# Kernel optimization log

Measured on AMD Instinct MI355X. Metric: run time of the kernel, lower is better.

The kernel has to match this reference:

```python
import jax, jax.numpy as jnp
import numpy as np

IMG_H, IMG_W = 800, 1216
STRIDES = [4, 8, 16, 32, 64]
SIZES = [32, 64, 128, 256, 512]
RATIOS = (2.0, 1.0, 0.5)
LVTOP = 1000     # per-level top-k
IMTOP = 1000     # image-level top-k
IOU_THR = 0.7
MIN_SIZE = 0.001
BBOX_CLIP = float(np.log(1000.0 / 16.0))  # dw/dh clamp, matches decode=(1,1,log(1000/16))


def conv2d(x, w, b, pad):
    y = jax.lax.conv_general_dilated(x, w, (1, 1), [(pad, pad), (pad, pad)],
                                     dimension_numbers=('NCHW', 'OIHW', 'NCHW'))
    return y + b[None, :, None, None]


def head_level(x, conv_w, conv_b, cls_w, cls_b, reg_w, reg_b):
    # ConvUnit 3x3 + plain ReLU (no BN), then 1x1 reg/cls heads
    B = x.shape[0]
    h = jax.nn.relu(conv2d(x, conv_w, conv_b, 1))
    reg = conv2d(h, reg_w, reg_b, 0).transpose(0, 2, 3, 1).reshape(B, -1, 4)      # [B,H*W*A,4]
    scr = jax.nn.sigmoid(conv2d(h, cls_w, cls_b, 0).transpose(0, 2, 3, 1).reshape(B, -1))  # [B,H*W*A]
    return reg, scr


def make_priors(H, W, stride, size):
    # rounded base anchors (1 scale x 3 ratios), corner-aligned grid (xyxy)
    r = jnp.array(RATIOS, dtype=jnp.float32)
    hr = jnp.sqrt(r)
    ws, hs = size / hr, size * hr
    base = jnp.round(jnp.stack([-ws / 2, -hs / 2, ws / 2, hs / 2], axis=1))  # [A,4]
    ys, xs = jnp.meshgrid(jnp.arange(H) * stride, jnp.arange(W) * stride, indexing='ij')
    shift = jnp.stack([xs, ys, xs, ys], -1).reshape(-1, 1, 4).astype(jnp.float32)
    return (shift + base[None]).reshape(-1, 4)  # [H*W*A,4], order matches head reshape


def decode(reg, priors):
    pw = priors[..., 2] - priors[..., 0]
    ph = priors[..., 3] - priors[..., 1]
    pcx = priors[..., 0] + 0.5 * pw
    pcy = priors[..., 1] + 0.5 * ph
    dx, dy = reg[..., 0], reg[..., 1]
    dw = jnp.minimum(reg[..., 2], BBOX_CLIP)
    dh = jnp.minimum(reg[..., 3], BBOX_CLIP)
    cx, cy = dx * pw + pcx, dy * ph + pcy
    w, h = jnp.exp(dw) * pw, jnp.exp(dh) * ph
    return jnp.stack([cx - 0.5 * w, cy - 0.5 * h, cx + 0.5 * w, cy + 0.5 * h], -1)


def nms_keep(boxes, scores):
    # greedy NMS; boxes [K,4] sorted by score desc, scores < -0.5 mark invalid/padding
    K = boxes.shape[0]
    area = (boxes[:, 2] - boxes[:, 0]) * (boxes[:, 3] - boxes[:, 1])
    lt = jnp.maximum(boxes[:, None, :2], boxes[None, :, :2])
    rb = jnp.minimum(boxes[:, None, 2:], boxes[None, :, 2:])
    wh = jnp.clip(rb - lt, 0.0)
    inter = wh[..., 0] * wh[..., 1]
    iou = inter / jnp.maximum(area[:, None] + area[None, :] - inter, 1e-9)
    iou = jax.lax.stop_gradient(iou)  # selection is discrete
    idx = jnp.arange(K)

    def step(keep, xs):
        row, i = xs
        sup = keep[i] & (row > IOU_THR) & (idx > i)
        return keep & ~sup, None

    keep, _ = jax.lax.scan(step, scores > -0.5, (iou, idx))
    return keep


def process_level(reg, scr, priors):
    B, N = scr.shape
    k = min(LVTOP, N)
    topv, topi = jax.lax.top_k(scr, k)                              # [B,k], sorted desc
    reg_s = jnp.take_along_axis(reg, topi[..., None], axis=1)       # [B,k,4]
    boxes = decode(reg_s, priors[topi])
    boxes = jnp.stack([
        jnp.clip(boxes[..., 0], 0.0, IMG_W), jnp.clip(boxes[..., 1], 0.0, IMG_H),
        jnp.clip(boxes[..., 2], 0.0, IMG_W), jnp.clip(boxes[..., 3], 0.0, IMG_H)], -1)
    w = boxes[..., 2] - boxes[..., 0]
    h = boxes[..., 3] - boxes[..., 1]
    sc = jnp.where((w > MIN_SIZE) & (h > MIN_SIZE), topv, -1.0)     # drop tiny boxes
    if k < LVTOP:  # pad small levels (e.g. P6) to a fixed candidate count
        boxes = jnp.pad(boxes, ((0, 0), (0, LVTOP - k), (0, 0)))
        sc = jnp.pad(sc, ((0, 0), (0, LVTOP - k)), constant_values=-1.0)
    keep = jax.vmap(nms_keep)(boxes, sc)                            # per-level NMS
    return boxes, jnp.where(keep, sc, -1.0)


def forward(p2, p3, p4, p5, p6, conv_w, conv_b, cls_w, cls_b, reg_w, reg_b):
    levels = [p2, p3, p4, p5, p6]
    all_boxes, all_scores = [], []
    for lvl, stride, size in zip(levels, STRIDES, SIZES):
        reg, scr = head_level(lvl, conv_w, conv_b, cls_w, cls_b, reg_w, reg_b)
        priors = make_priors(lvl.shape[2], lvl.shape[3], stride, size)
        b, s = process_level(reg, scr, priors)
        all_boxes.append(b)
        all_scores.append(s)
    boxes = jnp.concatenate(all_boxes, axis=1)
    scores = jnp.concatenate(all_scores, axis=1)
    fv, fi = jax.lax.top_k(scores, IMTOP)                           # image-level top-k
    fb = jnp.take_along_axis(boxes, fi[..., None], axis=1)
    return jnp.concatenate([fb, fv[..., None]], axis=-1)            # [B, IMTOP, 5]


def setup_inputs():
    key = jax.random.key(0)
    ks = jax.random.split(key, 8)
    C = 256
    shapes = [(2, C, 200, 304), (2, C, 100, 152), (2, C, 50, 76), (2, C, 25, 38), (2, C, 13, 19)]
    inp = {}
    for i, (name, sh) in enumerate(zip(['p2', 'p3', 'p4', 'p5', 'p6'], shapes)):
        inp[name] = jax.random.normal(ks[i], sh, dtype=jnp.float32)
    inp['conv_w'] = jax.random.normal(ks[5], (C, C, 3, 3), dtype=jnp.float32) * 0.02
    inp['conv_b'] = jnp.zeros((C,), dtype=jnp.float32)
    inp['cls_w'] = jax.random.normal(ks[6], (3, C, 1, 1), dtype=jnp.float32) * 0.02
    inp['cls_b'] = jnp.zeros((3,), dtype=jnp.float32)
    inp['reg_w'] = jax.random.normal(ks[7], (12, C, 1, 1), dtype=jnp.float32) * 0.01
    inp['reg_b'] = jnp.zeros((12,), dtype=jnp.float32)
    return inp


def reference(p2, p3, p4, p5, p6, conv_w, conv_b, cls_w, cls_b, reg_w, reg_b):
    return forward(p2, p3, p4, p5, p6, conv_w, conv_b, cls_w, cls_b, reg_w, reg_b)
```

## Files before the change

### kernel.cpp

```cpp
#include <hip/hip_runtime.h>
#include <stdint.h>
#include <math.h>

typedef unsigned long long u64;
typedef unsigned int u32;
typedef unsigned char u8;
typedef short s16x8 __attribute__((ext_vector_type(8)));
typedef float f32x4 __attribute__((ext_vector_type(4)));

#define ATOT 242991
#define PXTOT 80997
#define PXPAD 82971

__device__ __constant__ int    d_Hs[5]      = {200,100,50,25,13};
__device__ __constant__ int    d_Ws[5]      = {304,152,76,38,19};
__device__ __constant__ int    d_Wp[5]      = {306,154,78,40,21};
__device__ __constant__ int    d_stridec[5] = {4,8,16,32,64};
__device__ __constant__ double d_sized[5]   = {32.0,64.0,128.0,256.0,512.0};
__device__ __constant__ int    d_off[5]     = {0,182400,228000,239400,242250};
__device__ __constant__ int    d_pxoff[6]   = {0,60800,76000,79800,80750,80997};
__device__ __constant__ int    d_poff[5]    = {0,61812,77520,81576,82656};
__device__ __constant__ int    d_Ncand[5]   = {182400,45600,11400,2850,741};
__device__ __constant__ int    d_xcb[5]     = {0,1900,2375,2494,2524};
__device__ __constant__ int    d_ctb[5]     = {0,1000,1300,1400,1425};
__device__ __constant__ int    d_tX[5]      = {5,3,2,1,1};

__device__ __forceinline__ u32 f2k32(float f) {
  u32 u = __float_as_uint(f);
  return (u & 0x80000000u) ? ~u : (u | 0x80000000u);
}
__device__ __forceinline__ float k2f32(u32 k) {
  u32 u = (k & 0x80000000u) ? (k & 0x7FFFFFFFu) : ~k;
  return __uint_as_float(u);
}
__device__ __forceinline__ u64 d2k(double d) {
  u64 b = (u64)__double_as_longlong(d);
  return (b & 0x8000000000000000ull) ? ~b : (b | 0x8000000000000000ull);
}
__device__ __forceinline__ unsigned short f2bf(float v) {
  u32 b = __float_as_uint(v);
  return (unsigned short)((b + 0x7FFFu + ((b >> 16) & 1u)) >> 16);
}
__device__ __forceinline__ float bf2f(unsigned short h) {
  return __uint_as_float(((u32)h) << 16);
}

__global__ void wtrans_k(const float* __restrict__ w, float* __restrict__ wt) {
  int gid = blockIdx.x * 256 + threadIdx.x;
  if (gid >= 2304 * 256) return;
  int oc = gid & 255;
  int rest = gid >> 8;
  int ic = rest / 9, tap = rest % 9;
  wt[gid] = w[(oc * 256 + ic) * 9 + tap];
}

__global__ void wcvt_k(const float* __restrict__ w, short* __restrict__ wbh,
                       short* __restrict__ wbl) {
  int gid = blockIdx.x * 256 + threadIdx.x;
  if (gid >= 73728) return;
  int lane = gid & 63;
  int rest = gid >> 6;
  int oct = rest & 15, rs = rest >> 4;
  int slice = rs & 7, tap = rs >> 3;
  int oc = oct * 16 + (lane & 15);
  int icb = slice * 32 + (lane >> 4) * 8;
  size_t ob = (size_t)gid * 8;
#pragma unroll
  for (int j = 0; j < 8; ++j) {
    float v = w[(oc * 256 + icb + j) * 9 + tap];
    unsigned short h = f2bf(v);
    wbh[ob + j] = (short)h;
    wbl[ob + j] = (short)f2bf(v - bf2f(h));
  }
}

__global__ __launch_bounds__(256) void xcvt_k(
    const float* __restrict__ x0, const float* __restrict__ x1,
    const float* __restrict__ x2, const float* __restrict__ x3,
    const float* __restrict__ x4, short* __restrict__ xh, short* __restrict__ xl)
{
  __shared__ float tile[32 * 257];
  const int bid = blockIdx.x;
  const int b = bid / 2532;
  int r = bid % 2532;
  int lvl = 0;
#pragma unroll
  for (int l2 = 1; l2 < 5; ++l2) if (r >= d_xcb[l2]) lvl = l2;
  const int chunk = r - d_xcb[lvl];
  const int H = d_Hs[lvl], W = d_Ws[lvl], HW = H * W, Wp = d_Wp[lvl];
  const int px0 = chunk * 32;
  const float* xs[5] = {x0, x1, x2, x3, x4};
  const float* xb = xs[lvl] + (size_t)b * 256 * HW;
  const int t = threadIdx.x;

  for (int icg = 0; icg < 32; ++icg) {
    int ic = icg * 8 + (t >> 5);
    int px = px0 + (t & 31);
    float v = (px < HW) ? xb[(size_t)ic * HW + px] : 0.f;
    tile[(t & 31) * 257 + ic] = v;
  }
  __syncthreads();
  int px = t >> 3;
  int gpx = px0 + px;
  if (gpx < HW) {
    int yy = gpx / W, xx = gpx % W;
    size_t obase = ((size_t)(b * PXPAD + d_poff[lvl]) +
                    (size_t)(yy + 1) * Wp + (xx + 1)) * 256 + (size_t)(t & 7) * 32;
#pragma unroll
    for (int q = 0; q < 4; ++q) {
      s16x8 hi, lo;
#pragma unroll
      for (int j = 0; j < 8; ++j) {
        u32 bits = __float_as_uint(tile[px * 257 + (t & 7) * 32 + q * 8 + j]);
        hi[j] = (short)(bits >> 16);
        lo[j] = (short)(bits & 0xFFFFu);
      }
      *(s16x8*)(xh + obase + q * 8) = hi;
      *(s16x8*)(xl + obase + q * 8) = lo;
    }
  }
}

__global__ __launch_bounds__(256) void conv_mfma_k(
    const short* __restrict__ xh,
    const short* __restrict__ wbh, const short* __restrict__ wbl,
    const float* __restrict__ convb, const float* __restrict__ clsw,
    const float* __restrict__ clsb, float* __restrict__ scr32)
{
  __shared__ float zl[4][64][3];
  const int bid = blockIdx.x;
  const int b = bid / 1438;
  int r = bid % 1438;
  int lvl = 0;
#pragma unroll
  for (int l2 = 1; l2 < 5; ++l2) if (r >= d_ctb[l2]) lvl = l2;
  const int lid = r - d_ctb[lvl];
  const int tX = d_tX[lvl];
  const int y = lid / tX, x0 = (lid % tX) * 64;
  const int W = d_Ws[lvl], Wp = d_Wp[lvl];
  const size_t pbase = (size_t)(b * PXPAD + d_poff[lvl]);

  const int t = threadIdx.x;
  const int lane = t & 63;
  const int wid = t >> 6;
  const int aoff = (lane & 15) * 256 + (lane >> 4) * 8;

  f32x4 acc[4][4];
#pragma unroll
  for (int m = 0; m < 4; ++m)
#pragma unroll
    for (int o = 0; o < 4; ++o) acc[m][o] = (f32x4){0.f, 0.f, 0.f, 0.f};

#pragma unroll 1
  for (int tap = 0; tap < 9; ++tap) {
    const int ky = tap / 3, kx = tap % 3;
    const size_t re = (pbase + (size_t)(y + ky) * Wp + (x0 + kx)) * 256;
    const short* pa = xh + re;
    const short* pbh = wbh + (size_t)tap * 8 * 16 * 512;
    const short* pbl = wbl + (size_t)tap * 8 * 16 * 512;
#pragma unroll 1
    for (int slice = 0; slice < 8; ++slice) {
      s16x8 bh[4], bl4[4], a[4];
#pragma unroll
      for (int o = 0; o < 4; ++o) {
        size_t bo = ((size_t)(slice * 16 + wid * 4 + o) * 64 + lane) * 8;
        bh[o]  = *(const s16x8*)(pbh + bo);
        bl4[o] = *(const s16x8*)(pbl + bo);
      }
#pragma unroll
      for (int m = 0; m < 4; ++m) {
        size_t ao = (size_t)aoff + slice * 32 + m * 4096;
        a[m] = *(const s16x8*)(pa + ao);
      }
#pragma unroll
      for (int m = 0; m < 4; ++m)
#pragma unroll
        for (int o = 0; o < 4; ++o) {
          acc[m][o] = __builtin_amdgcn_mfma_f32_16x16x32_bf16(a[m], bh[o],  acc[m][o], 0, 0, 0);
          acc[m][o] = __builtin_amdgcn_mfma_f32_16x16x32_bf16(a[m], bl4[o], acc[m][o], 0, 0, 0);
        }
    }
  }

  float bb[4], cw0[4], cw1[4], cw2[4];
#pragma unroll
  for (int o = 0; o < 4; ++o) {
    int oc = wid * 64 + o * 16 + (lane & 15);
    bb[o]  = convb[oc];
    cw0[o] = clsw[0 * 256 + oc];
    cw1[o] = clsw[1 * 256 + oc];
    cw2[o] = clsw[2 * 256 + oc];
  }
#pragma unroll
  for (int m = 0; m < 4; ++m) {
#pragma unroll
    for (int q = 0; q < 4; ++q) {
      float h0 = fmaxf(acc[m][0][q] + bb[0], 0.f);
      float h1 = fmaxf(acc[m][1][q] + bb[1], 0.f);
      float h2 = fmaxf(acc[m][2][q] + bb[2], 0.f);
      float h3 = fmaxf(acc[m][3][q] + bb[3], 0.f);
      float z0 = fmaf(h0, cw0[0], fmaf(h1, cw0[1], fmaf(h2, cw0[2], h3 * cw0[3])));
      float z1 = fmaf(h0, cw1[0], fmaf(h1, cw1[1], fmaf(h2, cw1[2], h3 * cw1[3])));
      float z2 = fmaf(h0, cw2[0], fmaf(h1, cw2[1], fmaf(h2, cw2[2], h3 * cw2[3])));
      z0 += __shfl_xor(z0, 1); z0 += __shfl_xor(z0, 2); z0 += __shfl_xor(z0, 4); z0 += __shfl_xor(z0, 8);
      z1 += __shfl_xor(z1, 1); z1 += __shfl_xor(z1, 2); z1 += __shfl_xor(z1, 4); z1 += __shfl_xor(z1, 8);
      z2 += __shfl_xor(z2, 1); z2 += __shfl_xor(z2, 2); z2 += __shfl_xor(z2, 4); z2 += __shfl_xor(z2, 8);
      if ((lane & 15) == 0) {
        int slot = m * 16 + (lane >> 4) * 4 + q;
        zl[wid][slot][0] = z0; zl[wid][slot][1] = z1; zl[wid][slot][2] = z2;
      }
    }
  }
  __syncthreads();
  if (t < 192) {
    int slot = t / 3, head = t % 3;
    int col = x0 + slot;
    if (col < W) {
      float z = zl[0][slot][head] + zl[1][slot][head] + zl[2][slot][head] +
                zl[3][slot][head] + clsb[head];
      int pix = y * W + col;
      scr32[(size_t)b * ATOT + d_off[lvl] + (size_t)pix * 3 + head] =
          1.f / (1.f + expf(-z));
    }
  }
}

__device__ __forceinline__ void locate(int gid, int& b, int& r, int& lvl) {
  b = gid / ATOT; r = gid % ATOT;
  lvl = (r < 182400) ? 0 : (r < 228000) ? 1 : (r < 239400) ? 2 : (r < 242250) ? 3 : 4;
}

__global__ void hist_hi_k(const float* __restrict__ scr, u32* __restrict__ hist) {
  int gid = blockIdx.x * 256 + threadIdx.x;
  if (gid >= 2 * ATOT) return;
  int b, r, lvl; locate(gid, b, r, lvl);
  u32 key = f2k32(scr[gid]);
  atomicAdd(&hist[((b * 5 + lvl) << 16) + (key >> 16)], 1u);
}

__global__ void scan_hi_k(const u32* __restrict__ hist, int* __restrict__ meta) {
  int bl = blockIdx.x, lvl = bl % 5;
  u32 k_sel = (u32)min(1000, d_Ncand[lvl]);
  const u32* h = hist + ((size_t)bl << 16);
  __shared__ u32 part[256];
  __shared__ u32 row[256];
  __shared__ int csel;
  __shared__ u32 cumsh;
  int t = threadIdx.x;
  u32 s = 0;
  for (int v = 0; v < 256; ++v) s += h[t * 256 + v];
  part[t] = s;
  __syncthreads();
  if (t == 0) {
    u32 cum = 0; int c = 255;
    for (; c > 0; --c) { if (cum + part[c] >= k_sel) break; cum += part[c]; }
    csel = c; cumsh = cum;
  }
  __syncthreads();
  row[t] = h[csel * 256 + t];
  __syncthreads();
  if (t == 0) {
    u32 cum = cumsh;
    int pivot = csel * 256;
    for (int v = 255; v >= 0; --v) {
      if (cum + row[v] >= k_sel) { pivot = csel * 256 + v; break; }
      cum += row[v];
    }
    meta[bl * 8 + 0] = pivot;
    meta[bl * 8 + 1] = (int)cum;
  }
}

__global__ void hist_lo_k(const float* __restrict__ scr, const int* __restrict__ meta,
                          u32* __restrict__ hist) {
  int gid = blockIdx.x * 256 + threadIdx.x;
  if (gid >= 2 * ATOT) return;
  int b, r, lvl; locate(gid, b, r, lvl);
  int bl = b * 5 + lvl;
  u32 key = f2k32(scr[gid]);
  if ((int)(key >> 16) == meta[bl * 8 + 0])
    atomicAdd(&hist[(bl << 16) + (key & 0xFFFFu)], 1u);
}

__global__ void scan_lo_k(const u32* __restrict__ hist, int* __restrict__ meta) {
  int bl = blockIdx.x, lvl = bl % 5;
  u32 k_sel = (u32)min(1000, d_Ncand[lvl]);
  const u32* h = hist + ((size_t)bl << 16);
  __shared__ u32 part[256];
  __shared__ u32 row[256];
  __shared__ int csel;
  __shared__ u32 cumsh;
  int t = threadIdx.x;
  u32 s = 0;
  for (int v = 0; v < 256; ++v) s += h[t * 256 + v];
  part[t] = s;
  __syncthreads();
  if (t == 0) {
    u32 cum = (u32)meta[bl * 8 + 1];
    int c = 255;
    for (; c > 0; --c) { if (cum + part[c] >= k_sel) break; cum += part[c]; }
    csel = c; cumsh = cum;
  }
  __syncthreads();
  row[t] = h[csel * 256 + t];
  __syncthreads();
  if (t == 0) {
    u32 cum = cumsh;
    int pivot = csel * 256;
    for (int v = 255; v >= 0; --v) {
      if (cum + row[v] >= k_sel) { pivot = csel * 256 + v; break; }
      cum += row[v];
    }
    u32 P = (((u32)meta[bl * 8 + 0]) << 16) | (u32)pivot;
    u32 T = f2k32(k2f32(P) - 5e-3f);
    if (d_Ncand[lvl] <= 1000) T = 0;
    meta[bl * 8 + 2] = (int)T;
    meta[bl * 8 + 4] = 0;
  }
}

__global__ void compact_k(const float* __restrict__ scr, int* __restrict__ meta,
                          u32* __restrict__ complist, u8* __restrict__ flags) {
  int gid = blockIdx.x * 256 + threadIdx.x;
  if (gid >= 2 * ATOT) return;
  int b, r, lvl; locate(gid, b, r, lvl);
  int bl = b * 5 + lvl;
  u32 key = f2k32(scr[gid]);
  if (key >= (u32)meta[bl * 8 + 2]) {
    int pos = atomicAdd(&meta[bl * 8 + 4], 1);
    if (pos < 8192) {
      u32 li = (u32)(r - d_off[lvl]);
      complist[bl * 8192 + pos] = li;
      flags[b * PXTOT + d_pxoff[lvl] + li / 3] = 1;
    }
  }
}

__global__ void pxcompact_k(u8* __restrict__ flags, u32* __restrict__ worklist,
                            int* __restrict__ wlcount) {
  int gid = blockIdx.x * 256 + threadIdx.x;
  if (gid >= 2 * PXTOT) return;
  if (flags[gid]) {
    flags[gid] = 0;
    int pos = atomicAdd(wlcount, 1);
    if (pos < 65536) worklist[pos] = (u32)gid;
  }
}

#define RSG 2048
__global__ __launch_bounds__(256) void rescore_k(
    const short* __restrict__ xh, const short* __restrict__ xl,
    const float* __restrict__ wt, const float* __restrict__ convb,
    const float* __restrict__ clsw, const float* __restrict__ clsb,
    const float* __restrict__ regw, const float* __restrict__ regb,
    const u32* __restrict__ worklist, const int* __restrict__ wlcount,
    double* __restrict__ scr64, double* __restrict__ reg64)
{
  __shared__ float xlb[4 * 2304];
  __shared__ double hl[4 * 256];
  const int t = threadIdx.x;
  int count = *wlcount; if (count > 65536) count = 65536;

  for (int base = blockIdx.x * 4; base < count; base += RSG * 4) {
    int sb[4], slvl[4], spix[4];
    size_t pb0[4];
    bool valid[4];
#pragma unroll
    for (int s = 0; s < 4; ++s) {
      int w = base + s;
      valid[s] = (w < count);
      sb[s] = 0; slvl[s] = 0; spix[s] = 0; pb0[s] = 0;
      if (valid[s]) {
        u32 g = worklist[w];
        int b = (int)(g / PXTOT), lp = (int)(g % PXTOT);
        int lvl = 0;
#pragma unroll
        for (int l = 1; l < 5; ++l) if (lp >= d_pxoff[l]) lvl = l;
        int pix = lp - d_pxoff[lvl];
        int W = d_Ws[lvl], Wp = d_Wp[lvl];
        int py = pix / W, px = pix % W;
        sb[s] = b; slvl[s] = lvl; spix[s] = pix;
        pb0[s] = ((size_t)(b * PXPAD + d_poff[lvl]) + (size_t)py * Wp + px) * 256;
      }
    }
    __syncthreads();
#pragma unroll
    for (int s = 0; s < 4; ++s) {
      if (valid[s]) {
        int Wp = d_Wp[slvl[s]];
        for (int i = t; i < 1152; i += 256) {
          int tap = i >> 7, pair = i & 127;
          int ky = tap / 3, kx = tap % 3;
          size_t po = pb0[s] + ((size_t)ky * Wp + kx) * 256 + (size_t)pair * 2;
          u32 vh = *(const u32*)(xh + po);
          u32 vl = *(const u32*)(xl + po);
          float xa  = __uint_as_float(((vh & 0xFFFFu) << 16) | (vl & 0xFFFFu));
          float xb2 = __uint_as_float((vh & 0xFFFF0000u) | (vl >> 16));
          xlb[s * 2304 + (pair * 2) * 9 + tap] = xa;
          xlb[s * 2304 + (pair * 2 + 1) * 9 + tap] = xb2;
        }
      }
    }
    __syncthreads();
    double h[4] = {0.0, 0.0, 0.0, 0.0};
    for (int ic = 0; ic < 256; ++ic) {
      double wd[9];
#pragma unroll
      for (int tap = 0; tap < 9; ++tap)
        wd[tap] = (double)wt[(ic * 9 + tap) * 256 + t];
#pragma unroll
      for (int s = 0; s < 4; ++s) {
        const float* xp = &xlb[s * 2304 + ic * 9];
#pragma unroll
        for (int tap = 0; tap < 9; ++tap)
          h[s] = fma((double)xp[tap], wd[tap], h[s]);
      }
    }
    double bias = (double)convb[t];
#pragma unroll
    for (int s = 0; s < 4; ++s) {
      h[s] = fmax(h[s] + bias, 0.0);
      hl[s * 256 + t] = h[s];
    }
    __syncthreads();
    {
      int s = t >> 6, lane = t & 63;
      if (valid[s]) {
        int lvl = slvl[s];
        size_t g3 = (size_t)sb[s] * ATOT + d_off[lvl] + (size_t)spix[s] * 3;
        for (int head = 0; head < 15; ++head) {
          const float* hw = (head < 3) ? (clsw + head * 256) : (regw + (head - 3) * 256);
          double part = 0.0;
#pragma unroll
          for (int q = 0; q < 4; ++q) {
            int oc = lane + q * 64;
            part = fma(hl[s * 256 + oc], (double)hw[oc], part);
          }
          part += __shfl_xor(part, 32);
          part += __shfl_xor(part, 16);
          part += __shfl_xor(part, 8);
          part += __shfl_xor(part, 4);
          part += __shfl_xor(part, 2);
          part += __shfl_xor(part, 1);
          if (lane == 0) {
            double z = part + (double)((head < 3) ? clsb[head] : regb[head - 3]);
            if (head < 3) scr64[g3 + head] = 1.0 / (1.0 + exp(-z));
            else { int hh = head - 3; reg64[(g3 + (hh >> 2)) * 4 + (hh & 3)] = z; }
          }
        }
      }
    }
    __syncthreads();
  }
}

__global__ void buildkeys_k(const u32* __restrict__ complist, const int* __restrict__ meta,
                            const double* __restrict__ scr64, u64* __restrict__ comp64) {
  int bl = blockIdx.x;
  int b = bl / 5, lvl = bl % 5;
  int M = meta[bl * 8 + 4]; if (M > 8192) M = 8192;
  for (int i = threadIdx.x; i < 8192; i += 256) {
    u64 key = 0;
    if (i < M) {
      u32 li = complist[bl * 8192 + i];
      double sc = scr64[(size_t)b * ATOT + d_off[lvl] + li];
      key = ((d2k(sc) >> 18) << 18) | (u64)(0x3FFFFu - li);
    }
    comp64[bl * 8192 + i] = key;
  }
}

__device__ void bitonic8192_desc(u64* s) {
  int t = threadIdx.x;
  for (int k = 2; k <= 8192; k <<= 1) {
    for (int j = k >> 1; j > 0; j >>= 1) {
      __syncthreads();
#pragma unroll
      for (int q = 0; q < 4; ++q) {
        int i = t + q * 1024;
        int l = (i << 1) - (i & (j - 1));
        int m = l + j;
        bool up = ((l & k) == 0);
        u64 a = s[l], bb = s[m];
        if ((a < bb) == up) { s[l] = bb; s[m] = a; }
      }
    }
  }
  __syncthreads();
}

__global__ __launch_bounds__(1024) void sort_level_k(const u64* __restrict__ comp64,
                                                     const int* __restrict__ meta,
                                                     int* __restrict__ topidx) {
  int bl = blockIdx.x, lvl = bl % 5;
  int k_sel = min(1000, d_Ncand[lvl]);
  __shared__ u64 s[8192];
  int M = meta[bl * 8 + 4]; if (M > 8192) M = 8192;
  for (int i = threadIdx.x; i < 8192; i += 1024)
    s[i] = (i < M) ? comp64[bl * 8192 + i] : 0ull;
  __syncthreads();
  bitonic8192_desc(s);
  for (int r = threadIdx.x; r < 1000; r += 1024) {
    int v = -1;
    if (r < k_sel && r < M) v = (int)(0x3FFFFu - (u32)(s[r] & 0x3FFFFu));
    topidx[bl * 1000 + r] = v;
  }
}

__global__ void decode_k(const int* __restrict__ topidx, const double* __restrict__ scr64,
                         const double* __restrict__ reg64, double* __restrict__ boxes,
                         double* __restrict__ sc0) {
  int gid = blockIdx.x * 256 + threadIdx.x;
  if (gid >= 10000) return;
  int bl = gid / 1000, rank = gid % 1000;
  int b = bl / 5, lvl = bl % 5;
  int idx = topidx[bl * 1000 + rank];
  double X1 = 0.0, Y1 = 0.0, X2 = 0.0, Y2 = 0.0, sc = -1.0;
  if (idx >= 0) {
    size_t g = (size_t)b * ATOT + d_off[lvl] + idx;
    double s = scr64[g];
    double dx = reg64[g * 4 + 0], dy = reg64[g * 4 + 1];
    const double BCLIP = 4.135166556742356;
    double dw = fmin(reg64[g * 4 + 2], BCLIP);
    double dh = fmin(reg64[g * 4 + 3], BCLIP);
    int a = idx % 3, pix = idx / 3;
    int W = d_Ws[lvl];
    int py = pix / W, px = pix % W;
    double r = (a == 0) ? 2.0 : (a == 1) ? 1.0 : 0.5;
    double hr = sqrt(r);
    double size = d_sized[lvl];
    double wsz = size / hr, hsz = size * hr;
    double bx2 = rint(wsz * 0.5), by2 = rint(hsz * 0.5);
    double bx1 = rint(-(wsz * 0.5)), by1 = rint(-(hsz * 0.5));
    double sx = (double)(px * d_stridec[lvl]), sy = (double)(py * d_stridec[lvl]);
    double x1 = sx + bx1, yy1 = sy + by1;
    double x2 = sx + bx2, yy2 = sy + by2;
    double pw = x2 - x1, ph = yy2 - yy1;
    double pcx = x1 + 0.5 * pw, pcy = yy1 + 0.5 * ph;
    double cx = dx * pw + pcx, cy = dy * ph + pcy;
    double w = exp(dw) * pw, h = exp(dh) * ph;
    X1 = fmin(fmax(cx - 0.5 * w, 0.0), 1216.0);
    Y1 = fmin(fmax(cy - 0.5 * h, 0.0), 800.0);
    X2 = fmin(fmax(cx + 0.5 * w, 0.0), 1216.0);
    Y2 = fmin(fmax(cy + 0.5 * h, 0.0), 800.0);
    sc = ((X2 - X1) > 0.001 && (Y2 - Y1) > 0.001) ? s : -1.0;
  }
  double* bp = boxes + (size_t)(bl * 1000 + rank) * 4;
  bp[0] = X1; bp[1] = Y1; bp[2] = X2; bp[3] = Y2;
  sc0[bl * 1000 + rank] = sc;
}

__global__ __launch_bounds__(256) void nms_mask_k(const double* __restrict__ boxes,
                                                  u64* __restrict__ gmask) {
  int blk = blockIdx.x;
  int bl = blk >> 2, qt = blk & 3;
  __shared__ double X1[1000], Y1[1000], X2[1000], Y2[1000], AR[1000];
  int t = threadIdx.x;
  for (int i = t; i < 1000; i += 256) {
    const double* bp = boxes + (size_t)(bl * 1000 + i) * 4;
    double x1 = bp[0], y1 = bp[1], x2 = bp[2], y2 = bp[3];
    X1[i] = x1; Y1[i] = y1; X2[i] = x2; Y2[i] = y2;
    AR[i] = (x2 - x1) * (y2 - y1);
  }
  __syncthreads();
  if (t < 250) {
    int i = qt * 250 + t;
    double ax1 = X1[i], ay1 = Y1[i], ax2 = X2[i], ay2 = Y2[i], aa = AR[i];
    u64* gm = gmask + (size_t)bl * 16000 + (size_t)i * 16;
    for (int wj = 0; wj < 16; ++wj) {
      u64 bits = 0;
      int jb0 = wj * 64;
      for (int jb = 0; jb < 64; ++jb) {
        int j = jb0 + jb;
        if (j <= i || j >= 1000) continue;
        double lx = fmax(ax1, X1[j]), ly = fmax(ay1, Y1[j]);
        double rx = fmin(ax2, X2[j]), ry = fmin(ay2, Y2[j]);
        double ww = fmax(rx - lx, 0.0), hh = fmax(ry - ly, 0.0);
        double inter = ww * hh;
        double uni = (aa + AR[j]) - inter;
        double iou = inter / fmax(uni, 1e-9);
        if (iou > 0.7) bits |= (1ull << jb);
      }
      gm[wj] = bits;
    }
  }
}

__global__ void nms_scan_k(double* __restrict__ sc0, const u64* __restrict__ gmask) {
  int bl = blockIdx.x;
  int lane = threadIdx.x;
  const u64* gm = gmask + (size_t)bl * 16000;
  u64 keepw = 0;
  if (lane < 16) {
    for (int jb = 0; jb < 64; ++jb) {
      int j = lane * 64 + jb;
      if (j < 1000 && sc0[bl * 1000 + j] > -0.5) keepw |= (1ull << jb);
    }
  }
  u64 m0 = 0, m1 = 0, m2 = 0, m3 = 0;
  if (lane < 16) {
    m0 = gm[0 * 16 + lane]; m1 = gm[1 * 16 + lane];
    m2 = gm[2 * 16 + lane]; m3 = gm[3 * 16 + lane];
  }
  for (int i = 0; i < 1000; i += 4) {
    u64 n0 = 0, n1 = 0, n2 = 0, n3 = 0;
    if (lane < 16 && i + 4 < 1000) {
      n0 = gm[(i + 4) * 16 + lane]; n1 = gm[(i + 5) * 16 + lane];
      n2 = gm[(i + 6) * 16 + lane]; n3 = gm[(i + 7) * 16 + lane];
    }
    { u64 kw = __shfl(keepw, (i    ) >> 6); if ((kw >> ((i    ) & 63)) & 1) { if (lane < 16) keepw &= ~m0; } }
    { u64 kw = __shfl(keepw, (i + 1) >> 6); if ((kw >> ((i + 1) & 63)) & 1) { if (lane < 16) keepw &= ~m1; } }
    { u64 kw = __shfl(keepw, (i + 2) >> 6); if ((kw >> ((i + 2) & 63)) & 1) { if (lane < 16) keepw &= ~m2; } }
    { u64 kw = __shfl(keepw, (i + 3) >> 6); if ((kw >> ((i + 3) & 63)) & 1) { if (lane < 16) keepw &= ~m3; } }
    m0 = n0; m1 = n1; m2 = n2; m3 = n3;
  }
  if (lane < 16) {
    for (int jb = 0; jb < 64; ++jb) {
      int j = lane * 64 + jb;
      if (j < 1000) {
        double ss = sc0[bl * 1000 + j];
        sc0[bl * 1000 + j] = ((keepw >> jb) & 1) ? ss : -1.0;
      }
    }
  }
}

__global__ __launch_bounds__(1024) void final_k(const double* __restrict__ sc0,
                                                const double* __restrict__ boxes,
                                                float* __restrict__ out) {
  int b = blockIdx.x;
  __shared__ u64 s[8192];
  for (int i = threadIdx.x; i < 8192; i += 1024) {
    u64 v = 0;
    if (i < 5000) {
      u64 k = d2k(sc0[b * 5000 + i]);
      v = ((k >> 18) << 18) | (u64)(0x3FFFFu - (u32)i);
    }
    s[i] = v;
  }
  __syncthreads();
  bitonic8192_desc(s);
  for (int r = threadIdx.x; r < 1000; r += 1024) {
    u64 v = s[r];
    int idx = (int)(0x3FFFFu - (u32)(v & 0x3FFFFu));
    double score = sc0[b * 5000 + idx];
    const double* bp = boxes + (size_t)(b * 5000 + idx) * 4;
    float* op = out + ((size_t)b * 1000 + r) * 5;
    op[0] = (float)bp[0]; op[1] = (float)bp[1];
    op[2] = (float)bp[2]; op[3] = (float)bp[3];
    op[4] = (float)score;
  }
}

extern "C" void kernel_launch(void* const* d_in, const int* in_sizes, int n_in,
                              void* d_out, int out_size, void* d_ws, size_t ws_size,
                              hipStream_t stream) {
  const float* p[5];
  for (int i = 0; i < 5; ++i) p[i] = (const float*)d_in[i];
  const float* conv_w = (const float*)d_in[5];
  const float* conv_b = (const float*)d_in[6];
  const float* cls_w  = (const float*)d_in[7];
  const float* cls_b  = (const float*)d_in[8];
  const float* reg_w  = (const float*)d_in[9];
  const float* reg_b  = (const float*)d_in[10];
  float* out = (float*)d_out;

  char* ws = (char*)d_ws;
  size_t off = 0;
  auto alloc = [&](size_t bytes) -> void* {
    void* pt = ws + off;
    off = (off + bytes + 255) & ~(size_t)255;
    return pt;
  };
  const size_t XTB = (size_t)2 * PXPAD * 256 * 2 + 65536;
  float*  wt       = (float*) alloc(2304ull * 256 * 4);
  short*  wbh      = (short*) alloc(73728ull * 8 * 2);
  short*  wbl      = (short*) alloc(73728ull * 8 * 2);
  short*  xh       = (short*) alloc(XTB);
  short*  xl       = (short*) alloc(XTB);
  float*  scr32    = (float*) alloc(2ull * ATOT * 4);
  double* scr64    = (double*)alloc(2ull * ATOT * 8);
  double* reg64    = (double*)alloc(2ull * ATOT * 4 * 8);
  u32*    hist     = (u32*)   alloc(10ull * 65536 * 4);
  int*    meta     = (int*)   alloc(10ull * 8 * 4);
  u32*    complist = (u32*)   alloc(10ull * 8192 * 4);
  u64*    comp64   = (u64*)   alloc(10ull * 8192 * 8);
  u8*     flags    = (u8*)    alloc(2ull * PXTOT);
  u32*    worklist = (u32*)   alloc(65536ull * 4);
  int*    wlcount  = (int*)   alloc(256);
  int*    topidx   = (int*)   alloc(10ull * 1000 * 4);
  double* boxes    = (double*)alloc(2ull * 5000 * 4 * 8);
  double* sc0      = (double*)alloc(2ull * 5000 * 8);
  u64*    gmask    = (u64*)   alloc(10ull * 1000 * 16 * 8);

  wtrans_k<<<(2304 * 256 + 255) / 256, 256, 0, stream>>>(conv_w, wt);
  wcvt_k<<<288, 256, 0, stream>>>(conv_w, wbh, wbl);
  hipMemsetAsync(xh, 0, XTB, stream);
  hipMemsetAsync(xl, 0, XTB, stream);
  xcvt_k<<<5064, 256, 0, stream>>>(p[0], p[1], p[2], p[3], p[4], xh, xl);
  conv_mfma_k<<<2876, 256, 0, stream>>>(xh, wbh, wbl, conv_b, cls_w, cls_b, scr32);

  int nblk = (2 * ATOT + 255) / 256;
  hipMemsetAsync(hist, 0, 10ull * 65536 * 4, stream);
  hist_hi_k<<<nblk, 256, 0, stream>>>(scr32, hist);
  scan_hi_k<<<10, 256, 0, stream>>>(hist, meta);
  hipMemsetAsync(hist, 0, 10ull * 65536 * 4, stream);
  hist_lo_k<<<nblk, 256, 0, stream>>>(scr32, meta, hist);
  scan_lo_k<<<10, 256, 0, stream>>>(hist, meta);

  hipMemsetAsync(flags, 0, 2ull * PXTOT, stream);
  hipMemsetAsync(wlcount, 0, 4, stream);
  compact_k<<<nblk, 256, 0, stream>>>(scr32, meta, complist, flags);
  pxcompact_k<<<(2 * PXTOT + 255) / 256, 256, 0, stream>>>(flags, worklist, wlcount);

  rescore_k<<<RSG, 256, 0, stream>>>(xh, xl, wt, conv_b, cls_w, cls_b, reg_w, reg_b,
                                     worklist, wlcount, scr64, reg64);

  buildkeys_k<<<10, 256, 0, stream>>>(complist, meta, scr64, comp64);
  sort_level_k<<<10, 1024, 0, stream>>>(comp64, meta, topidx);
  decode_k<<<40, 256, 0, stream>>>(topidx, scr64, reg64, boxes, sc0);
  nms_mask_k<<<40, 256, 0, stream>>>(boxes, gmask);
  nms_scan_k<<<10, 64, 0, stream>>>(sc0, gmask);
  final_k<<<2, 1024, 0, stream>>>(sc0, boxes, out);
}
```

Measured before the change: 2.160 ms.

## Drop bf16 low-part weight MFMAs, zero only borders, replicate histograms, size sort adaptively

The conv screening pass now uses only the high bf16 part of the weights, which halves the MFMA count and the weight loads. The full memsets of the padded activation buffers are replaced by a kernel that zeroes only the halo pixels. The score histograms are split into four replicas to reduce atomic contention, and the per-level bitonic sort runs on 2048 elements when the candidate count allows. Screening is less precise, which relies on the later fp64 rescore to keep the selection correct. The xcvt channel interleaving is also changed to give more coalesced stores.

```diff
diff --git a/kernel.cpp b/kernel.cpp
--- a/kernel.cpp
+++ b/kernel.cpp
@@ -24,6 +24,7 @@
 __device__ __constant__ int    d_xcb[5]     = {0,1900,2375,2494,2524};
 __device__ __constant__ int    d_ctb[5]     = {0,1000,1300,1400,1425};
 __device__ __constant__ int    d_tX[5]      = {5,3,2,1,1};
+__device__ __constant__ int    d_bcum[6]    = {0,1012,1520,1776,1906,1974};
 
 __device__ __forceinline__ u32 f2k32(float f) {
   u32 u = __float_as_uint(f);
@@ -40,9 +41,6 @@
 __device__ __forceinline__ unsigned short f2bf(float v) {
   u32 b = __float_as_uint(v);
   return (unsigned short)((b + 0x7FFFu + ((b >> 16) & 1u)) >> 16);
-}
-__device__ __forceinline__ float bf2f(unsigned short h) {
-  return __uint_as_float(((u32)h) << 16);
 }
 
 __global__ void wtrans_k(const float* __restrict__ w, float* __restrict__ wt) {
@@ -54,8 +52,7 @@
   wt[gid] = w[(oc * 256 + ic) * 9 + tap];
 }
 
-__global__ void wcvt_k(const float* __restrict__ w, short* __restrict__ wbh,
-                       short* __restrict__ wbl) {
+__global__ void wcvt_k(const float* __restrict__ w, short* __restrict__ wbh) {
   int gid = blockIdx.x * 256 + threadIdx.x;
   if (gid >= 73728) return;
   int lane = gid & 63;
@@ -66,11 +63,33 @@
   int icb = slice * 32 + (lane >> 4) * 8;
   size_t ob = (size_t)gid * 8;
 #pragma unroll
-  for (int j = 0; j < 8; ++j) {
-    float v = w[(oc * 256 + icb + j) * 9 + tap];
-    unsigned short h = f2bf(v);
-    wbh[ob + j] = (short)h;
-    wbl[ob + j] = (short)f2bf(v - bf2f(h));
+  for (int j = 0; j < 8; ++j)
+    wbh[ob + j] = (short)f2bf(w[(oc * 256 + icb + j) * 9 + tap]);
+}
+
+__global__ void border_zero_k(short* __restrict__ xh, short* __restrict__ xl) {
+  int tid = blockIdx.x * 256 + threadIdx.x;
+  if (tid >= 2 * 1974 * 8) return;
+  int oct = tid & 7;
+  int rest = tid >> 3;
+  int b = rest / 1974;
+  int bi = rest % 1974;
+  int lvl = 0;
+#pragma unroll
+  for (int l = 1; l < 5; ++l) if (bi >= d_bcum[l]) lvl = l;
+  int li = bi - d_bcum[lvl];
+  int W = d_Ws[lvl], H = d_Hs[lvl], Wp = d_Wp[lvl];
+  int py, px;
+  if (li < Wp)            { py = 0;     px = li; }
+  else if (li < 2 * Wp)   { py = H + 1; px = li - Wp; }
+  else { int rem = li - 2 * Wp; py = 1 + rem / 2; px = (rem & 1) ? (W + 1) : 0; }
+  size_t base = ((size_t)(b * PXPAD + d_poff[lvl]) + (size_t)py * Wp + px) * 256
+              + (size_t)oct * 32;
+  s16x8 z = (s16x8){0,0,0,0,0,0,0,0};
+#pragma unroll
+  for (int j = 0; j < 4; ++j) {
+    *(s16x8*)(xh + base + j * 8) = z;
+    *(s16x8*)(xl + base + j * 8) = z;
   }
 }
 
@@ -100,30 +119,30 @@
     tile[(t & 31) * 257 + ic] = v;
   }
   __syncthreads();
-  int px = t >> 3;
+  int px = t >> 3, sub = t & 7;
   int gpx = px0 + px;
   if (gpx < HW) {
     int yy = gpx / W, xx = gpx % W;
-    size_t obase = ((size_t)(b * PXPAD + d_poff[lvl]) +
-                    (size_t)(yy + 1) * Wp + (xx + 1)) * 256 + (size_t)(t & 7) * 32;
+    size_t pxbase = ((size_t)(b * PXPAD + d_poff[lvl]) +
+                     (size_t)(yy + 1) * Wp + (xx + 1)) * 256;
 #pragma unroll
     for (int q = 0; q < 4; ++q) {
+      int ch0 = q * 64 + sub * 8;
       s16x8 hi, lo;
 #pragma unroll
       for (int j = 0; j < 8; ++j) {
-        u32 bits = __float_as_uint(tile[px * 257 + (t & 7) * 32 + q * 8 + j]);
+        u32 bits = __float_as_uint(tile[px * 257 + ch0 + j]);
         hi[j] = (short)(bits >> 16);
         lo[j] = (short)(bits & 0xFFFFu);
       }
-      *(s16x8*)(xh + obase + q * 8) = hi;
-      *(s16x8*)(xl + obase + q * 8) = lo;
+      *(s16x8*)(xh + pxbase + ch0) = hi;
+      *(s16x8*)(xl + pxbase + ch0) = lo;
     }
   }
 }
 
 __global__ __launch_bounds__(256) void conv_mfma_k(
-    const short* __restrict__ xh,
-    const short* __restrict__ wbh, const short* __restrict__ wbl,
+    const short* __restrict__ xh, const short* __restrict__ wbh,
     const float* __restrict__ convb, const float* __restrict__ clsw,
     const float* __restrict__ clsb, float* __restrict__ scr32)
 {
@@ -157,15 +176,13 @@
     const size_t re = (pbase + (size_t)(y + ky) * Wp + (x0 + kx)) * 256;
     const short* pa = xh + re;
     const short* pbh = wbh + (size_t)tap * 8 * 16 * 512;
-    const short* pbl = wbl + (size_t)tap * 8 * 16 * 512;
 #pragma unroll 1
     for (int slice = 0; slice < 8; ++slice) {
-      s16x8 bh[4], bl4[4], a[4];
+      s16x8 bh[4], a[4];
 #pragma unroll
       for (int o = 0; o < 4; ++o) {
         size_t bo = ((size_t)(slice * 16 + wid * 4 + o) * 64 + lane) * 8;
-        bh[o]  = *(const s16x8*)(pbh + bo);
-        bl4[o] = *(const s16x8*)(pbl + bo);
+        bh[o] = *(const s16x8*)(pbh + bo);
       }
 #pragma unroll
       for (int m = 0; m < 4; ++m) {
@@ -175,10 +192,8 @@
 #pragma unroll
       for (int m = 0; m < 4; ++m)
 #pragma unroll
-        for (int o = 0; o < 4; ++o) {
-          acc[m][o] = __builtin_amdgcn_mfma_f32_16x16x32_bf16(a[m], bh[o],  acc[m][o], 0, 0, 0);
-          acc[m][o] = __builtin_amdgcn_mfma_f32_16x16x32_bf16(a[m], bl4[o], acc[m][o], 0, 0, 0);
-        }
+        for (int o = 0; o < 4; ++o)
+          acc[m][o] = __builtin_amdgcn_mfma_f32_16x16x32_bf16(a[m], bh[o], acc[m][o], 0, 0, 0);
     }
   }
 
@@ -235,20 +250,24 @@
   if (gid >= 2 * ATOT) return;
   int b, r, lvl; locate(gid, b, r, lvl);
   u32 key = f2k32(scr[gid]);
-  atomicAdd(&hist[((b * 5 + lvl) << 16) + (key >> 16)], 1u);
+  int rep = blockIdx.x & 3;
+  atomicAdd(&hist[((((b * 5 + lvl) << 2) | rep) << 16) + (key >> 16)], 1u);
 }
 
 __global__ void scan_hi_k(const u32* __restrict__ hist, int* __restrict__ meta) {
   int bl = blockIdx.x, lvl = bl % 5;
   u32 k_sel = (u32)min(1000, d_Ncand[lvl]);
-  const u32* h = hist + ((size_t)bl << 16);
+  const u32* h = hist + ((size_t)bl << 18);
   __shared__ u32 part[256];
   __shared__ u32 row[256];
   __shared__ int csel;
   __shared__ u32 cumsh;
   int t = threadIdx.x;
   u32 s = 0;
-  for (int v = 0; v < 256; ++v) s += h[t * 256 + v];
+  for (int v = 0; v < 256; ++v) {
+    int idx = t * 256 + v;
+    s += h[idx] + h[65536 + idx] + h[131072 + idx] + h[196608 + idx];
+  }
   part[t] = s;
   __syncthreads();
   if (t == 0) {
@@ -257,7 +276,10 @@
     csel = c; cumsh = cum;
   }
   __syncthreads();
-  row[t] = h[csel * 256 + t];
+  {
+    int idx = csel * 256 + t;
+    row[t] = h[idx] + h[65536 + idx] + h[131072 + idx] + h[196608 + idx];
+  }
   __syncthreads();
   if (t == 0) {
     u32 cum = cumsh;
@@ -278,21 +300,26 @@
   int b, r, lvl; locate(gid, b, r, lvl);
   int bl = b * 5 + lvl;
   u32 key = f2k32(scr[gid]);
-  if ((int)(key >> 16) == meta[bl * 8 + 0])
-    atomicAdd(&hist[(bl << 16) + (key & 0xFFFFu)], 1u);
+  if ((int)(key >> 16) == meta[bl * 8 + 0]) {
+    int rep = blockIdx.x & 3;
+    atomicAdd(&hist[(((bl << 2) | rep) << 16) + (key & 0xFFFFu)], 1u);
+  }
 }
 
 __global__ void scan_lo_k(const u32* __restrict__ hist, int* __restrict__ meta) {
   int bl = blockIdx.x, lvl = bl % 5;
   u32 k_sel = (u32)min(1000, d_Ncand[lvl]);
-  const u32* h = hist + ((size_t)bl << 16);
+  const u32* h = hist + ((size_t)bl << 18);
   __shared__ u32 part[256];
   __shared__ u32 row[256];
   __shared__ int csel;
   __shared__ u32 cumsh;
   int t = threadIdx.x;
   u32 s = 0;
-  for (int v = 0; v < 256; ++v) s += h[t * 256 + v];
+  for (int v = 0; v < 256; ++v) {
+    int idx = t * 256 + v;
+    s += h[idx] + h[65536 + idx] + h[131072 + idx] + h[196608 + idx];
+  }
   part[t] = s;
   __syncthreads();
   if (t == 0) {
@@ -302,7 +329,10 @@
     csel = c; cumsh = cum;
   }
   __syncthreads();
-  row[t] = h[csel * 256 + t];
+  {
+    int idx = csel * 256 + t;
+    row[t] = h[idx] + h[65536 + idx] + h[131072 + idx] + h[196608 + idx];
+  }
   __syncthreads();
   if (t == 0) {
     u32 cum = cumsh;
@@ -470,14 +500,12 @@
   }
 }
 
-__device__ void bitonic8192_desc(u64* s) {
+__device__ void bitonic_desc_n(u64* s, int SZ) {
   int t = threadIdx.x;
-  for (int k = 2; k <= 8192; k <<= 1) {
+  for (int k = 2; k <= SZ; k <<= 1) {
     for (int j = k >> 1; j > 0; j >>= 1) {
       __syncthreads();
-#pragma unroll
-      for (int q = 0; q < 4; ++q) {
-        int i = t + q * 1024;
+      for (int i = t; i < (SZ >> 1); i += 1024) {
         int l = (i << 1) - (i & (j - 1));
         int m = l + j;
         bool up = ((l & k) == 0);
@@ -496,10 +524,11 @@
   int k_sel = min(1000, d_Ncand[lvl]);
   __shared__ u64 s[8192];
   int M = meta[bl * 8 + 4]; if (M > 8192) M = 8192;
-  for (int i = threadIdx.x; i < 8192; i += 1024)
+  int SZ = (M <= 2048) ? 2048 : 8192;
+  for (int i = threadIdx.x; i < SZ; i += 1024)
     s[i] = (i < M) ? comp64[bl * 8192 + i] : 0ull;
   __syncthreads();
-  bitonic8192_desc(s);
+  bitonic_desc_n(s, SZ);
   for (int r = threadIdx.x; r < 1000; r += 1024) {
     int v = -1;
     if (r < k_sel && r < M) v = (int)(0x3FFFFu - (u32)(s[r] & 0x3FFFFu));
@@ -639,7 +668,7 @@
     s[i] = v;
   }
   __syncthreads();
-  bitonic8192_desc(s);
+  bitonic_desc_n(s, 8192);
   for (int r = threadIdx.x; r < 1000; r += 1024) {
     u64 v = s[r];
     int idx = (int)(0x3FFFFu - (u32)(v & 0x3FFFFu));
@@ -675,13 +704,12 @@
   const size_t XTB = (size_t)2 * PXPAD * 256 * 2 + 65536;
   float*  wt       = (float*) alloc(2304ull * 256 * 4);
   short*  wbh      = (short*) alloc(73728ull * 8 * 2);
-  short*  wbl      = (short*) alloc(73728ull * 8 * 2);
   short*  xh       = (short*) alloc(XTB);
   short*  xl       = (short*) alloc(XTB);
   float*  scr32    = (float*) alloc(2ull * ATOT * 4);
   double* scr64    = (double*)alloc(2ull * ATOT * 8);
   double* reg64    = (double*)alloc(2ull * ATOT * 4 * 8);
-  u32*    hist     = (u32*)   alloc(10ull * 65536 * 4);
+  u32*    hist     = (u32*)   alloc(40ull * 65536 * 4);
   int*    meta     = (int*)   alloc(10ull * 8 * 4);
   u32*    complist = (u32*)   alloc(10ull * 8192 * 4);
   u64*    comp64   = (u64*)   alloc(10ull * 8192 * 8);
@@ -694,17 +722,16 @@
   u64*    gmask    = (u64*)   alloc(10ull * 1000 * 16 * 8);
 
   wtrans_k<<<(2304 * 256 + 255) / 256, 256, 0, stream>>>(conv_w, wt);
-  wcvt_k<<<288, 256, 0, stream>>>(conv_w, wbh, wbl);
-  hipMemsetAsync(xh, 0, XTB, stream);
-  hipMemsetAsync(xl, 0, XTB, stream);
+  wcvt_k<<<288, 256, 0, stream>>>(conv_w, wbh);
+  border_zero_k<<<(2 * 1974 * 8 + 255) / 256, 256, 0, stream>>>(xh, xl);
   xcvt_k<<<5064, 256, 0, stream>>>(p[0], p[1], p[2], p[3], p[4], xh, xl);
-  conv_mfma_k<<<2876, 256, 0, stream>>>(xh, wbh, wbl, conv_b, cls_w, cls_b, scr32);
+  conv_mfma_k<<<2876, 256, 0, stream>>>(xh, wbh, conv_b, cls_w, cls_b, scr32);
 
   int nblk = (2 * ATOT + 255) / 256;
-  hipMemsetAsync(hist, 0, 10ull * 65536 * 4, stream);
+  hipMemsetAsync(hist, 0, 40ull * 65536 * 4, stream);
   hist_hi_k<<<nblk, 256, 0, stream>>>(scr32, hist);
   scan_hi_k<<<10, 256, 0, stream>>>(hist, meta);
-  hipMemsetAsync(hist, 0, 10ull * 65536 * 4, stream);
+  hipMemsetAsync(hist, 0, 40ull * 65536 * 4, stream);
   hist_lo_k<<<nblk, 256, 0, stream>>>(scr32, meta, hist);
   scan_lo_k<<<10, 256, 0, stream>>>(hist, meta);
 
```

Result: faster. 1.869 ms (-13.5%).
